# Performance work log

Measured on AMD Instinct MI355X. Metric: run time of the kernel, lower is better.

## Reference

```python
import jax, jax.numpy as jnp
import numpy as np

N, E = 50000, 800000          # nodes, directed edges
IN_DIM, HC, OUT_DIM = 128, 64, 128
NEG_SLOPE = 0.2               # PyG GATConv default leaky_relu slope
EPS = 1e-5                    # PyG LayerNorm default eps


def setup_inputs() -> dict:
    key = jax.random.key(0)
    ks = jax.random.split(key, 10)
    s = 0.1
    return {
        "x": jax.random.normal(ks[0], (N, IN_DIM), jnp.float32),
        "edge_index": jax.random.randint(ks[1], (2, E), 0, N, dtype=jnp.int32),
        # conv1: GATConv(IN_DIM -> HC, heads=2, concat=True)
        "W1": jax.random.normal(ks[2], (IN_DIM, 2 * HC), jnp.float32) * s,
        "att_src1": jax.random.normal(ks[3], (2, HC), jnp.float32) * s,
        "att_dst1": jax.random.normal(ks[4], (2, HC), jnp.float32) * s,
        "b1": jnp.zeros((2 * HC,), jnp.float32),
        "ln1_w": jnp.ones((2 * HC,), jnp.float32),
        "ln1_b": jnp.zeros((2 * HC,), jnp.float32),
        # conv2: GATConv(2*HC -> OUT_DIM, heads=1, concat=False)
        "W2": jax.random.normal(ks[5], (2 * HC, OUT_DIM), jnp.float32) * s,
        "att_src2": jax.random.normal(ks[6], (1, OUT_DIM), jnp.float32) * s,
        "att_dst2": jax.random.normal(ks[7], (1, OUT_DIM), jnp.float32) * s,
        "b2": jnp.zeros((OUT_DIM,), jnp.float32),
        "ln2_w": jnp.ones((OUT_DIM,), jnp.float32),
        "ln2_b": jnp.zeros((OUT_DIM,), jnp.float32),
    }


def gat_conv(x, src, dst, W, att_src, att_dst, bias, heads, C, concat):
    """PyG GATConv (shared lin for src/dst, self-loops already in src/dst)."""
    n = x.shape[0]
    h = (x @ W).reshape(n, heads, C)                       # [N,H,C]
    a_src = jnp.einsum('nhc,hc->nh', h, att_src)           # [N,H]
    a_dst = jnp.einsum('nhc,hc->nh', h, att_dst)           # [N,H]
    e = jax.nn.leaky_relu(a_src[src] + a_dst[dst], NEG_SLOPE)   # [E',H]
    # numerically-stable softmax over incoming edges of each dst node
    emax = jax.ops.segment_max(e, dst, num_segments=n)     # [N,H] (self-loops => non-empty)
    ex = jnp.exp(e - emax[dst])
    denom = jax.ops.segment_sum(ex, dst, num_segments=n)
    alpha = ex / (denom[dst] + 1e-16)                      # [E',H]
    out = jax.ops.segment_sum(h[src] * alpha[:, :, None], dst, num_segments=n)  # [N,H,C]
    out = out.reshape(n, heads * C) if concat else out.mean(axis=1)
    return out + bias


def graph_layernorm(x, w, b):
    """PyG LayerNorm, mode='graph', single graph: normalize over ALL nodes+features."""
    mean = x.mean()
    xc = x - mean
    var = (xc * xc).mean()
    return xc * jax.lax.rsqrt(var + EPS) * w + b


def reference(x, edge_index, W1, att_src1, att_dst1, b1, ln1_w, ln1_b,
              W2, att_src2, att_dst2, b2, ln2_w, ln2_b):
    n = x.shape[0]
    loop = jnp.arange(n, dtype=edge_index.dtype)
    src = jnp.concatenate([edge_index[0], loop])           # add self-loops for GAT convs
    dst = jnp.concatenate([edge_index[1], loop])

    h = gat_conv(x, src, dst, W1, att_src1, att_dst1, b1, heads=2, C=HC, concat=True)
    h = jax.nn.relu(graph_layernorm(h, ln1_w, ln1_b))
    h = gat_conv(h, src, dst, W2, att_src2, att_dst2, b2, heads=1, C=OUT_DIM, concat=False)
    h = graph_layernorm(h, ln2_w, ln2_b)

    # SimpleConv(aggr='mean') over the ORIGINAL edges (no self-loops), then residual
    s0, d0 = edge_index[0], edge_index[1]
    agg = jax.ops.segment_sum(h[s0], d0, num_segments=n)
    cnt = jax.ops.segment_sum(jnp.ones(s0.shape, h.dtype), d0, num_segments=n)
    mean_agg = agg / jnp.maximum(cnt, 1.0)[:, None]
    return jax.nn.relu(mean_agg + x)
```

## Files before the change

### kernel.cpp

```cpp
#include <hip/hip_runtime.h>
#include <hip/hip_bf16.h>
#include <cstdint>
#include <cstddef>

#define NN 50000
#define EE 800000
#define DD 128
#define NEG 0.2f
#define EPSL 1e-5f

#define NB   64
#define EPB  12544
#define NBKT 196
#define HM   (NBKT * NB)
#define SCAP 7168

#define GROWS 64
#define AB    (NN / 8)

typedef __hip_bfloat16 bf16;
typedef short short8 __attribute__((ext_vector_type(8)));
typedef float f32x4 __attribute__((ext_vector_type(4)));

__device__ inline float bflo(unsigned u) { return __uint_as_float(u << 16); }
__device__ inline float bfhi(unsigned u) { return __uint_as_float(u & 0xffff0000u); }
__device__ inline float bf2f(unsigned short u) { return __uint_as_float((unsigned)u << 16); }

__device__ inline unsigned short f2bf(float f) {
    __bf16 h = (__bf16)f;
    return __builtin_bit_cast(unsigned short, h);
}
__device__ inline unsigned pack2(float a, float b) {
    return (unsigned)f2bf(a) | ((unsigned)f2bf(b) << 16);
}

__device__ inline void store4(float* Out, size_t idx, float4 v) {
    *(float4*)&Out[idx] = v;
}
__device__ inline void store4(bf16* Out, size_t idx, float4 v) {
    union { bf16 b[4]; ushort4 u; } cv;
    cv.b[0] = (bf16)v.x; cv.b[1] = (bf16)v.y; cv.b[2] = (bf16)v.z; cv.b[3] = (bf16)v.w;
    *(ushort4*)&Out[idx] = cv.u;
}


__global__ __launch_bounds__(256) void hist_kernel(const int* __restrict__ ei,
                                                   int* __restrict__ histG) {
    __shared__ int lh[NBKT];
    int tid = threadIdx.x;
    for (int t = tid; t < NBKT; t += 256) lh[t] = 0;
    __syncthreads();
    int base = blockIdx.x * EPB;
    #pragma unroll
    for (int j = 0; j < (EPB + 1023) / 1024; ++j) {
        int off = (j * 256 + tid) * 4;
        if (off < EPB) {
            int i4 = base + off;
            if (i4 < EE) {
                int4 d4 = *(const int4*)&ei[EE + i4];
                atomicAdd(&lh[(unsigned)d4.x >> 8], 1);
                atomicAdd(&lh[(unsigned)d4.y >> 8], 1);
                atomicAdd(&lh[(unsigned)d4.z >> 8], 1);
                atomicAdd(&lh[(unsigned)d4.w >> 8], 1);
            }
        }
    }
    __syncthreads();
    for (int t = tid; t < NBKT; t += 256) histG[t * NB + blockIdx.x] = lh[t];
}

__global__ __launch_bounds__(1024) void scan_hist_kernel(const int* __restrict__ histG,
                                                         int* __restrict__ offs,
                                                         int* __restrict__ bstart) {
    __shared__ int wsum[16];
    __shared__ int carry_s;
    int tid = threadIdx.x, lane = tid & 63, wv = tid >> 6;
    if (tid == 0) carry_s = 0;
    __syncthreads();
    for (int base = 0; base < HM; base += 4096) {
        int i4 = base + tid * 4;
        int4 v = make_int4(0, 0, 0, 0);
        if (i4 + 3 < HM) v = *(const int4*)&histG[i4];
        else {
            if (i4 + 0 < HM) v.x = histG[i4 + 0];
            if (i4 + 1 < HM) v.y = histG[i4 + 1];
            if (i4 + 2 < HM) v.z = histG[i4 + 2];
            if (i4 + 3 < HM) v.w = histG[i4 + 3];
        }
        int tsum = v.x + v.y + v.z + v.w;
        int x = tsum;
        for (int off = 1; off < 64; off <<= 1) {
            int t = __shfl_up(x, off);
            if (lane >= off) x += t;
        }
        if (lane == 63) wsum[wv] = x;
        __syncthreads();
        if (wv == 0) {
            int s = (lane < 16) ? wsum[lane] : 0;
            for (int off = 1; off < 16; off <<= 1) {
                int t = __shfl_up(s, off);
                if (lane >= off) s += t;
            }
            if (lane < 16) wsum[lane] = s;
        }
        __syncthreads();
        int waveoff = (wv == 0) ? 0 : wsum[wv - 1];
        int carry = carry_s;
        int o0 = carry + waveoff + x - tsum;
        int o1 = o0 + v.x, o2 = o1 + v.y, o3 = o2 + v.z;
        if (i4 + 3 < HM) *(int4*)&offs[i4] = make_int4(o0, o1, o2, o3);
        else {
            if (i4 + 0 < HM) offs[i4 + 0] = o0;
            if (i4 + 1 < HM) offs[i4 + 1] = o1;
            if (i4 + 2 < HM) offs[i4 + 2] = o2;
            if (i4 + 3 < HM) offs[i4 + 3] = o3;
        }
        if (i4 < HM && (i4 % NB) == 0) bstart[i4 / NB] = o0;
        __syncthreads();
        if (tid == 0) carry_s += wsum[15];
        __syncthreads();
    }
    if (tid == 0) bstart[NBKT] = carry_s;
}

__global__ __launch_bounds__(512) void bucket_sort_kernel(const unsigned* __restrict__ tmp,
                                                          const int* __restrict__ bstart,
                                                          unsigned* __restrict__ col,
                                                          int* __restrict__ row_ptr) {
    __shared__ int cnt[256];
    __shared__ int cpos[256];
    __shared__ int wtot[4];
    __shared__ unsigned stage[SCAP];
    __shared__ unsigned sorted[SCAP];
    int tid = threadIdx.x, lane = tid & 63, wv = tid >> 6;
    int s0 = bstart[blockIdx.x], s1 = bstart[blockIdx.x + 1];
    int cntE = s1 - s0;
    bool lds_ok = (cntE <= SCAP);
    for (int t = tid; t < 256; t += 512) cnt[t] = 0;
    __syncthreads();
    if (lds_ok) {
        for (int i = tid; i < cntE; i += 512) {
            unsigned k = tmp[s0 + i];
            stage[i] = k;
            atomicAdd(&cnt[(k >> 16) & 0xFF], 1);
        }
    } else {
        for (int i = s0 + tid; i < s1; i += 512)
            atomicAdd(&cnt[(tmp[i] >> 16) & 0xFF], 1);
    }
    __syncthreads();
    int v = 0, x = 0;
    if (tid < 256) {
        v = cnt[tid];
        x = v;
        for (int off = 1; off < 64; off <<= 1) {
            int t = __shfl_up(x, off);
            if (lane >= off) x += t;
        }
        if (lane == 63) wtot[wv] = x;
    }
    __syncthreads();
    if (tid < 256) {
        int add = 0;
        for (int k = 0; k < wv; ++k) add += wtot[k];
        int start = s0 + add + x - v;
        cpos[tid] = start;
        int d = blockIdx.x * 256 + tid;
        if (d <= NN) row_ptr[d] = start;
    }
    __syncthreads();
    if (lds_ok) {
        for (int i = tid; i < cntE; i += 512) {
            unsigned key = stage[i];
            int pos = atomicAdd(&cpos[(key >> 16) & 0xFF], 1);
            sorted[pos - s0] = key;
        }
        __syncthreads();
        for (int i = tid; i < cntE; i += 512) col[s0 + i] = sorted[i];
    } else {
        for (int i = s0 + tid; i < s1; i += 512) {
            unsigned key = tmp[i];
            int pos = atomicAdd(&cpos[(key >> 16) & 0xFF], 1);
            col[pos] = key;
        }
    }
}

template <int H, bool LN, typename XT>
__device__ __forceinline__ void gemm_attn_body(int gb,
                                               const XT* __restrict__ X,
                                               const float* __restrict__ W,
                                               const float* __restrict__ att_s,
                                               const float* __restrict__ att_d,
                                               const float2* __restrict__ pstats,
                                               const float* __restrict__ lnw,
                                               const float* __restrict__ lnb,
                                               bf16* __restrict__ Hout,
                                               float* __restrict__ a_src,
                                               float* __restrict__ a_dst) {
    __shared__ __align__(16) char lds[(128 * 136 + 64 * 136) * 2 + 2048];
    unsigned short* Bt = (unsigned short*)lds;
    unsigned short* As = (unsigned short*)(lds + 128 * 136 * 2);
    float* Cs = (float*)lds;
    float* psum = (float*)(lds + (128 * 136 + 64 * 136) * 2);
    __shared__ double w1d[8], w2d[8], sred[2];

    int tid = threadIdx.x;
    int lane = tid & 63, w = tid >> 6;
    int row0 = gb * GROWS;

    double s1 = 0.0, s2 = 0.0;
    if (LN) {
        for (int i = tid; i < AB; i += 512) {
            float2 pv = pstats[i];
            s1 += (double)pv.x; s2 += (double)pv.y;
        }
    }

    {
        int c = tid & 127, kg = tid >> 7;
        #pragma unroll 2
        for (int i = 0; i < 8; ++i) {
            int k0 = i * 16 + kg * 4;
            float wa = W[(size_t)(k0 + 0) * DD + c];
            float wb = W[(size_t)(k0 + 1) * DD + c];
            float wcv = W[(size_t)(k0 + 2) * DD + c];
            float wdv = W[(size_t)(k0 + 3) * DD + c];
            uint2 pk = make_uint2(pack2(wa, wb), pack2(wcv, wdv));
            *(uint2*)&Bt[c * 136 + k0] = pk;
        }
    }

    if (LN) {
        #pragma unroll
        for (int off = 32; off; off >>= 1) {
            s1 += __shfl_xor(s1, off);
            s2 += __shfl_xor(s2, off);
        }
        if (lane == 0) { w1d[w] = s1; w2d[w] = s2; }
    }
    __syncthreads();
    if (LN && tid == 0) {
        double a = 0.0, b = 0.0;
        #pragma unroll
        for (int k = 0; k < 8; ++k) { a += w1d[k]; b += w2d[k]; }
        sred[0] = a; sred[1] = b;
    }
    __syncthreads();

    {
        int sub = tid & 31, rq = tid >> 5;
        int c4 = sub * 4;
        float mean = 0.f, inv = 1.f;
        float4 lw4 = make_float4(1.f, 1.f, 1.f, 1.f), lb4 = make_float4(0.f, 0.f, 0.f, 0.f);
        if (LN) {
            const double M = (double)NN * DD;
            double mean_d = sred[0] / M;
            double var_d = sred[1] / M - mean_d * mean_d;
            mean = (float)mean_d;
            inv = rsqrtf((float)var_d + EPSL);
            lw4 = *(const float4*)&lnw[c4];
            lb4 = *(const float4*)&lnb[c4];
        }
        #pragma unroll
        for (int i = 0; i < 4; ++i) {
            int r = i * 16 + rq;
            int row = row0 + r;
            float4 xv = make_float4(0.f, 0.f, 0.f, 0.f);
            if (row < NN) {
                if constexpr (sizeof(XT) == 4) {
                    xv = *(const float4*)&((const float*)X)[(size_t)row * DD + c4];
                } else {
                    ushort4 xb = *(const ushort4*)&((const unsigned short*)X)[(size_t)row * DD + c4];
                    xv = make_float4(bf2f(xb.x), bf2f(xb.y), bf2f(xb.z), bf2f(xb.w));
                }
            }
            if (LN) {
                xv.x = fmaxf((xv.x - mean) * inv * lw4.x + lb4.x, 0.f);
                xv.y = fmaxf((xv.y - mean) * inv * lw4.y + lb4.y, 0.f);
                xv.z = fmaxf((xv.z - mean) * inv * lw4.z + lb4.z, 0.f);
                xv.w = fmaxf((xv.w - mean) * inv * lw4.w + lb4.w, 0.f);
            }
            uint2 pk = make_uint2(pack2(xv.x, xv.y), pack2(xv.z, xv.w));
            *(uint2*)&As[r * 136 + c4] = pk;
        }
    }
    __syncthreads();

    int rg = w & 3, cg = w >> 2;
    int l15 = lane & 15, quad = lane >> 4;
    f32x4 acc[4];
    #pragma unroll
    for (int t = 0; t < 4; ++t) acc[t] = 0.f;
    const unsigned short* Arow = As + (rg * 16 + l15) * 136 + quad * 8;
    const unsigned short* Brow = Bt + l15 * 136 + quad * 8;
    #pragma unroll
    for (int ks = 0; ks < 4; ++ks) {
        short8 a = *(const short8*)(Arow + ks * 32);
        #pragma unroll
        for (int tt = 0; tt < 4; ++tt) {
            short8 b = *(const short8*)(Brow + (cg * 4 + tt) * 16 * 136 + ks * 32);
            acc[tt] = __builtin_amdgcn_mfma_f32_16x16x32_bf16(a, b, acc[tt], 0, 0, 0);
        }
    }
    __syncthreads();

    #pragma unroll
    for (int tt = 0; tt < 4; ++tt)
        #pragma unroll
        for (int r = 0; r < 4; ++r)
            Cs[(rg * 16 + quad * 4 + r) * 132 + (cg * 4 + tt) * 16 + l15] = acc[tt][r];

    float ds[4] = {0.f, 0.f, 0.f, 0.f}, dd[4] = {0.f, 0.f, 0.f, 0.f};
    #pragma unroll
    for (int tt = 0; tt < 4; ++tt) {
        int cc = (cg * 4 + tt) * 16 + l15;
        float as_ = att_s[cc], ad_ = att_d[cc];
        #pragma unroll
        for (int r = 0; r < 4; ++r) {
            ds[r] = fmaf(acc[tt][r], as_, ds[r]);
            dd[r] = fmaf(acc[tt][r], ad_, dd[r]);
        }
    }
    #pragma unroll
    for (int off = 1; off < 16; off <<= 1) {
        #pragma unroll
        for (int r = 0; r < 4; ++r) {
            ds[r] += __shfl_xor(ds[r], off);
            dd[r] += __shfl_xor(dd[r], off);
        }
    }
    if (l15 == 0) {
        #pragma unroll
        for (int r = 0; r < 4; ++r) {
            int rr = rg * 16 + quad * 4 + r;
            int row = row0 + rr;
            if (H == 2) {
                if (row < NN) {
                    a_src[row * 2 + cg] = ds[r];
                    a_dst[row * 2 + cg] = dd[r];
                }
            } else {
                psum[cg * 64 + rr] = ds[r];
                psum[128 + cg * 64 + rr] = dd[r];
            }
        }
    }
    __syncthreads();

    if (H == 1 && tid < 64) {
        int row = row0 + tid;
        if (row < NN) {
            a_src[row] = psum[tid] + psum[64 + tid];
            a_dst[row] = psum[128 + tid] + psum[192 + tid];
        }
    }

    {
        int sub = tid & 31, rq = tid >> 5;
        int c4 = sub * 4;
        unsigned short* Hp = (unsigned short*)Hout;
        #pragma unroll
        for (int i = 0; i < 4; ++i) {
            int r = i * 16 + rq;
            int row = row0 + r;
            if (row < NN) {
                float4 cv = *(const float4*)&Cs[r * 132 + c4];
                ushort4 pk;
                pk.x = f2bf(cv.x); pk.y = f2bf(cv.y);
                pk.z = f2bf(cv.z); pk.w = f2bf(cv.w);
                *(ushort4*)&Hp[(size_t)row * DD + c4] = pk;
            }
        }
    }
}

template <int H, bool LN, typename XT>
__global__ __launch_bounds__(512) void gemm_attn(const XT* __restrict__ X,
                                                 const float* __restrict__ W,
                                                 const float* __restrict__ att_s,
                                                 const float* __restrict__ att_d,
                                                 const float2* __restrict__ pstats,
                                                 const float* __restrict__ lnw,
                                                 const float* __restrict__ lnb,
                                                 bf16* __restrict__ Hout,
                                                 float* __restrict__ a_src,
                                                 float* __restrict__ a_dst) {
    gemm_attn_body<H, LN, XT>(blockIdx.x, X, W, att_s, att_d, pstats, lnw, lnb,
                              Hout, a_src, a_dst);
}

__global__ __launch_bounds__(512) void scatter_gemm1(const int* __restrict__ ei,
                                                     const int* __restrict__ offs,
                                                     unsigned* __restrict__ tmp,
                                                     const float* __restrict__ X,
                                                     const float* __restrict__ W,
                                                     const float* __restrict__ att_s,
                                                     const float* __restrict__ att_d,
                                                     bf16* __restrict__ Hout,
                                                     float* __restrict__ a_src,
                                                     float* __restrict__ a_dst) {
    if (blockIdx.x < NB) {
        __shared__ int lofs[NBKT];
        int tid = threadIdx.x;
        for (int t = tid; t < NBKT; t += 512) lofs[t] = offs[t * NB + blockIdx.x];
        __syncthreads();
        int base = blockIdx.x * EPB;
        #pragma unroll
        for (int j = 0; j < (EPB + 2047) / 2048; ++j) {
            int off = (j * 512 + tid) * 4;
            if (off < EPB) {
                int i4 = base + off;
                if (i4 < EE) {
                    int4 s4 = *(const int4*)&ei[i4];
                    int4 d4 = *(const int4*)&ei[EE + i4];
                    unsigned k0 = ((unsigned)d4.x << 16) | (unsigned)s4.x;
                    unsigned k1 = ((unsigned)d4.y << 16) | (unsigned)s4.y;
                    unsigned k2 = ((unsigned)d4.z << 16) | (unsigned)s4.z;
                    unsigned k3 = ((unsigned)d4.w << 16) | (unsigned)s4.w;
                    tmp[atomicAdd(&lofs[(unsigned)d4.x >> 8], 1)] = k0;
                    tmp[atomicAdd(&lofs[(unsigned)d4.y >> 8], 1)] = k1;
                    tmp[atomicAdd(&lofs[(unsigned)d4.z >> 8], 1)] = k2;
                    tmp[atomicAdd(&lofs[(unsigned)d4.w >> 8], 1)] = k3;
                }
            }
        }
    } else {
        gemm_attn_body<2, false, float>(blockIdx.x - NB, X, W, att_s, att_d,
                                        nullptr, nullptr, nullptr, Hout, a_src, a_dst);
    }
}

template <int H, typename OT>
__global__ __launch_bounds__(256) void gat_agg(const int* __restrict__ row_ptr,
                                               const unsigned* __restrict__ col,
                                               const bf16* __restrict__ Hin,
                                               const float* __restrict__ a_src,
                                               const float* __restrict__ a_dst,
                                               const float* __restrict__ bias,
                                               OT* __restrict__ Out,
                                               float2* __restrict__ pstats) {
    int tid = threadIdx.x;
    int sl = tid & 31;
    int hw = tid >> 5;
    int n = blockIdx.x * 8 + hw;
    int c0 = sl * 4;
    const int head4 = (H == 2) ? (sl >> 4) : 0;

    int beg = row_ptr[n], end = row_ptr[n + 1];
    int deg = end - beg;

    float ad0 = a_dst[n * H + 0];
    float ad1 = (H == 2) ? a_dst[n * H + 1] : 0.f;
    const ushort* Hp = (const ushort*)Hin + c0;

    float acc[4] = {0.f, 0.f, 0.f, 0.f};
    float dl0 = 0.f, dl1 = 0.f;

    for (int base = 0; base < deg; base += 32) {
        int ecnt = min(32, deg - base);
        int sv = 0; float w0v = 0.f, w1v = 0.f;
        if (sl < ecnt) {
            sv = (int)(col[beg + base + sl] & 0xffffu);
            if (H == 2) {
                float2 av = *(const float2*)&a_src[sv * 2];
                float e0 = av.x + ad0; e0 = (e0 > 0.f) ? e0 : NEG * e0;
                float e1 = av.y + ad1; e1 = (e1 > 0.f) ? e1 : NEG * e1;
                w0v = __expf(e0); w1v = __expf(e1);
                dl0 += w0v; dl1 += w1v;
            } else {
                float e0 = a_src[sv] + ad0; e0 = (e0 > 0.f) ? e0 : NEG * e0;
                w0v = __expf(e0);
                dl0 += w0v;
            }
        }
        int ecnt16 = (ecnt + 15) & ~15;
        for (int j = 0; j < ecnt16; j += 16) {
            int s[16]; uint2 h[16]; float ww[16];
            #pragma unroll
            for (int u = 0; u < 16; ++u) s[u] = __shfl(sv, j + u, 32);
            #pragma unroll
            for (int u = 0; u < 16; ++u) h[u] = *(const uint2*)(Hp + (size_t)s[u] * DD);
            #pragma unroll
            for (int u = 0; u < 16; ++u) {
                if (H == 2) {
                    float a0 = __shfl(w0v, j + u, 32), b0 = __shfl(w1v, j + u, 32);
                    ww[u] = head4 ? b0 : a0;
                } else {
                    ww[u] = __shfl(w0v, j + u, 32);
                }
            }
            #pragma unroll
            for (int u = 0; u < 16; ++u) {
                acc[0] = fmaf(ww[u], bflo(h[u].x), acc[0]);
                acc[1] = fmaf(ww[u], bfhi(h[u].x), acc[1]);
                acc[2] = fmaf(ww[u], bflo(h[u].y), acc[2]);
                acc[3] = fmaf(ww[u], bfhi(h[u].y), acc[3]);
            }
        }
    }

    #pragma unroll
    for (int off = 1; off < 32; off <<= 1) {
        dl0 += __shfl_xor(dl0, off);
        if (H == 2) dl1 += __shfl_xor(dl1, off);
    }

    float e0 = a_src[n * H + 0] + ad0; e0 = (e0 > 0.f) ? e0 : NEG * e0;
    float ws0 = __expf(e0);
    float ws1 = 0.f;
    if (H == 2) {
        float e1 = a_src[n * H + 1] + ad1; e1 = (e1 > 0.f) ? e1 : NEG * e1;
        ws1 = __expf(e1);
    }
    float den = (H == 2 && head4) ? (dl1 + ws1) : (dl0 + ws0);
    float wself = (H == 2 && head4) ? ws1 : ws0;
    float rinv = 1.f / (den + 1e-16f);
    uint2 hs = *(const uint2*)(Hp + (size_t)n * DD);
    float4 bi = *(const float4*)&bias[c0];
    float4 o;
    o.x = fmaf(wself, bflo(hs.x), acc[0]) * rinv + bi.x;
    o.y = fmaf(wself, bfhi(hs.x), acc[1]) * rinv + bi.y;
    o.z = fmaf(wself, bflo(hs.y), acc[2]) * rinv + bi.z;
    o.w = fmaf(wself, bfhi(hs.y), acc[3]) * rinv + bi.w;
    store4(Out, (size_t)n * DD + c0, o);

    float t1 = o.x + o.y + o.z + o.w;
    float t2 = o.x * o.x + o.y * o.y + o.z * o.z + o.w * o.w;
    #pragma unroll
    for (int off = 1; off < 32; off <<= 1) {
        t1 += __shfl_xor(t1, off);
        t2 += __shfl_xor(t2, off);
    }
    __shared__ float2 ps[8];
    if (sl == 0) ps[hw] = make_float2(t1, t2);
    __syncthreads();
    if (tid == 0) {
        float a = 0.f, b = 0.f;
        #pragma unroll
        for (int k = 0; k < 8; ++k) { a += ps[k].x; b += ps[k].y; }
        pstats[blockIdx.x] = make_float2(a, b);
    }
}

__global__ __launch_bounds__(1024) void reduce_stats_kernel(const float2* __restrict__ pstats,
                                                            double* __restrict__ stats) {
    int tid = threadIdx.x, lane = tid & 63, wv = tid >> 6;
    double s1 = 0.0, s2 = 0.0;
    for (int i = tid; i < AB; i += 1024) {
        float2 v = pstats[i];
        s1 += (double)v.x; s2 += (double)v.y;
    }
    for (int off = 32; off; off >>= 1) {
        s1 += __shfl_xor(s1, off);
        s2 += __shfl_xor(s2, off);
    }
    __shared__ double w1[16], w2[16];
    if (lane == 0) { w1[wv] = s1; w2[wv] = s2; }
    __syncthreads();
    if (tid == 0) {
        double a = 0.0, b = 0.0;
        for (int i = 0; i < 16; ++i) { a += w1[i]; b += w2[i]; }
        stats[0] = a; stats[1] = b;
    }
}

__global__ __launch_bounds__(256) void simpleconv_kernel(const int* __restrict__ row_ptr,
                                                         const unsigned* __restrict__ col,
                                                         const bf16* __restrict__ Hin,
                                                         const float* __restrict__ X,
                                                         const double* __restrict__ stats,
                                                         const float* __restrict__ lnw,
                                                         const float* __restrict__ lnb,
                                                         float* __restrict__ Out) {
    int tid = threadIdx.x;
    int sl = tid & 31;
    int n = blockIdx.x * 8 + (tid >> 5);
    int c0 = sl * 4;
    int beg = row_ptr[n], end = row_ptr[n + 1];
    int deg = end - beg;
    const ushort* Hp = (const ushort*)Hin + c0;

    float acc[4] = {0.f, 0.f, 0.f, 0.f};
    for (int base = 0; base < deg; base += 32) {
        int ecnt = min(32, deg - base);
        int sv = 0;
        if (sl < ecnt) sv = (int)(col[beg + base + sl] & 0xffffu);
        int ecnt16 = (ecnt + 15) & ~15;
        for (int j = 0; j < ecnt16; j += 16) {
            int s[16]; uint2 h[16];
            #pragma unroll
            for (int u = 0; u < 16; ++u) s[u] = __shfl(sv, j + u, 32);
            #pragma unroll
            for (int u = 0; u < 16; ++u) h[u] = *(const uint2*)(Hp + (size_t)s[u] * DD);
            #pragma unroll
            for (int u = 0; u < 16; ++u) {
                float ww = (j + u < ecnt) ? 1.f : 0.f;
                acc[0] = fmaf(ww, bflo(h[u].x), acc[0]);
                acc[1] = fmaf(ww, bfhi(h[u].x), acc[1]);
                acc[2] = fmaf(ww, bflo(h[u].y), acc[2]);
                acc[3] = fmaf(ww, bfhi(h[u].y), acc[3]);
            }
        }
    }

    const double M = (double)NN * DD;
    double mean_d = stats[0] / M;
    double var_d = stats[1] / M - mean_d * mean_d;
    float mean2 = (float)mean_d;
    float inv2 = rsqrtf((float)var_d + EPSL);
    float rc = 1.f / (float)((deg > 0) ? deg : 1);
    float4 xr = *(const float4*)&X[(size_t)n * DD + c0];
    float4 o;
    if (deg > 0) {
        float4 lw = *(const float4*)&lnw[c0];
        float4 lb = *(const float4*)&lnb[c0];
        o.x = (acc[0] * rc - mean2) * inv2 * lw.x + lb.x;
        o.y = (acc[1] * rc - mean2) * inv2 * lw.y + lb.y;
        o.z = (acc[2] * rc - mean2) * inv2 * lw.z + lb.z;
        o.w = (acc[3] * rc - mean2) * inv2 * lw.w + lb.w;
    } else {
        o.x = o.y = o.z = o.w = 0.f;
    }
    o.x = fmaxf(o.x + xr.x, 0.f);
    o.y = fmaxf(o.y + xr.y, 0.f);
    o.z = fmaxf(o.z + xr.z, 0.f);
    o.w = fmaxf(o.w + xr.w, 0.f);
    *(float4*)&Out[(size_t)n * DD + c0] = o;
}

extern "C" void kernel_launch(void* const* d_in, const int* in_sizes, int n_in,
                              void* d_out, int out_size, void* d_ws, size_t ws_size,
                              hipStream_t stream) {
    const float* x    = (const float*)d_in[0];
    const int*   ei   = (const int*)d_in[1];
    const float* W1   = (const float*)d_in[2];
    const float* as1  = (const float*)d_in[3];
    const float* ad1  = (const float*)d_in[4];
    const float* b1   = (const float*)d_in[5];
    const float* ln1w = (const float*)d_in[6];
    const float* ln1b = (const float*)d_in[7];
    const float* W2   = (const float*)d_in[8];
    const float* as2  = (const float*)d_in[9];
    const float* ad2  = (const float*)d_in[10];
    const float* b2   = (const float*)d_in[11];
    const float* ln2w = (const float*)d_in[12];
    const float* ln2b = (const float*)d_in[13];
    float* out = (float*)d_out;

    char* p = (char*)d_ws;
    auto alloc = [&](size_t bytes) {
        void* r = (void*)p;
        p += (bytes + 255) & ~(size_t)255;
        return r;
    };
    unsigned* tmp     = (unsigned*)alloc((size_t)EE * 4);
    unsigned* col     = (unsigned*)alloc((size_t)EE * 4);
    int*      histG   = (int*)alloc((size_t)HM * 4);
    int*      offs    = (int*)alloc((size_t)HM * 4);
    int*      bstart  = (int*)alloc((size_t)(NBKT + 1) * 4);
    int*      row_ptr = (int*)alloc((size_t)(NN + 256) * 4);
    double*   stats2  = (double*)alloc(16);
    float2*   pstats  = (float2*)alloc((size_t)AB * 8);
    bf16*     bufA    = (bf16*)alloc((size_t)NN * DD * 2);
    bf16*     bufB    = (bf16*)alloc((size_t)NN * DD * 2);
    float*    aS1     = (float*)alloc((size_t)NN * 2 * 4);
    float*    aD1     = (float*)alloc((size_t)NN * 2 * 4);
    float*    aS2     = (float*)alloc((size_t)NN * 4);
    float*    aD2     = (float*)alloc((size_t)NN * 4);

    const int GB = (NN + GROWS - 1) / GROWS;

    hist_kernel<<<NB, 256, 0, stream>>>(ei, histG);
    scan_hist_kernel<<<1, 1024, 0, stream>>>(histG, offs, bstart);
    scatter_gemm1<<<NB + GB, 512, 0, stream>>>(ei, offs, tmp,
                                               x, W1, as1, ad1, bufA, aS1, aD1);
    bucket_sort_kernel<<<NBKT, 512, 0, stream>>>(tmp, bstart, col, row_ptr);

    gat_agg<2, bf16><<<AB, 256, 0, stream>>>(row_ptr, col, bufA, aS1, aD1, b1, bufB, pstats);

    gemm_attn<1, true, bf16><<<GB, 512, 0, stream>>>(bufB, W2, as2, ad2,
                                                     pstats, ln1w, ln1b,
                                                     bufA, aS2, aD2);
    gat_agg<1, bf16><<<AB, 256, 0, stream>>>(row_ptr, col, bufA, aS2, aD2, b2, bufB, pstats);
    reduce_stats_kernel<<<1, 1024, 0, stream>>>(pstats, stats2);

    simpleconv_kernel<<<AB, 256, 0, stream>>>(row_ptr, col, bufB, x,
                                              stats2, ln2w, ln2b, out);
}
```

Measured before the change: 265.2 us.

## Split aggregation kernels into channel halves with two edges per half-wave

The GAT aggregation and SimpleConv kernels now launch twice as many blocks. Each block covers one 64-channel half of the feature row, and each half-warp processes alternating edges. The two half-warp accumulators are combined with a shuffle at the end. The goal is more memory-level parallelism and occupancy for the gather-heavy edge loops, at the cost of reading the edge list and attention scores twice and doubling the partial-statistics buffer that the LayerNorm reductions consume.

```diff
diff --git a/kernel.cpp b/kernel.cpp
--- a/kernel.cpp
+++ b/kernel.cpp
@@ -211,7 +211,7 @@
 
     double s1 = 0.0, s2 = 0.0;
     if (LN) {
-        for (int i = tid; i < AB; i += 512) {
+        for (int i = tid; i < 2 * AB; i += 512) {
             float2 pv = pstats[i];
             s1 += (double)pv.x; s2 += (double)pv.y;
         }
@@ -443,90 +443,78 @@
     int tid = threadIdx.x;
     int sl = tid & 31;
     int hw = tid >> 5;
-    int n = blockIdx.x * 8 + hw;
-    int c0 = sl * 4;
-    const int head4 = (H == 2) ? (sl >> 4) : 0;
+    int ch = (blockIdx.x < AB) ? 0 : 1;
+    int blk = blockIdx.x - ch * AB;
+    int n = blk * 8 + hw;
+    int half = sl >> 4;
+    int c4 = ch * 64 + (sl & 15) * 4;
 
     int beg = row_ptr[n], end = row_ptr[n + 1];
     int deg = end - beg;
 
-    float ad0 = a_dst[n * H + 0];
-    float ad1 = (H == 2) ? a_dst[n * H + 1] : 0.f;
-    const ushort* Hp = (const ushort*)Hin + c0;
+    float ad = a_dst[n * H + ((H == 2) ? ch : 0)];
+    const ushort* Hp = (const ushort*)Hin + c4;
 
     float acc[4] = {0.f, 0.f, 0.f, 0.f};
-    float dl0 = 0.f, dl1 = 0.f;
+    float dl = 0.f;
 
     for (int base = 0; base < deg; base += 32) {
         int ecnt = min(32, deg - base);
-        int sv = 0; float w0v = 0.f, w1v = 0.f;
+        int sv = 0; float wv = 0.f;
         if (sl < ecnt) {
             sv = (int)(col[beg + base + sl] & 0xffffu);
-            if (H == 2) {
-                float2 av = *(const float2*)&a_src[sv * 2];
-                float e0 = av.x + ad0; e0 = (e0 > 0.f) ? e0 : NEG * e0;
-                float e1 = av.y + ad1; e1 = (e1 > 0.f) ? e1 : NEG * e1;
-                w0v = __expf(e0); w1v = __expf(e1);
-                dl0 += w0v; dl1 += w1v;
-            } else {
-                float e0 = a_src[sv] + ad0; e0 = (e0 > 0.f) ? e0 : NEG * e0;
-                w0v = __expf(e0);
-                dl0 += w0v;
-            }
+            float as_ = (H == 2) ? a_src[sv * 2 + ch] : a_src[sv];
+            float e = as_ + ad; e = (e > 0.f) ? e : NEG * e;
+            wv = __expf(e);
+            dl += wv;
         }
         int ecnt16 = (ecnt + 15) & ~15;
         for (int j = 0; j < ecnt16; j += 16) {
-            int s[16]; uint2 h[16]; float ww[16];
+            int s[8]; uint2 h[8]; float ww[8];
             #pragma unroll
-            for (int u = 0; u < 16; ++u) s[u] = __shfl(sv, j + u, 32);
+            for (int q = 0; q < 8; ++q) s[q] = __shfl(sv, j + 2 * q + half, 32);
             #pragma unroll
-            for (int u = 0; u < 16; ++u) h[u] = *(const uint2*)(Hp + (size_t)s[u] * DD);
+            for (int q = 0; q < 8; ++q) h[q] = *(const uint2*)(Hp + (size_t)s[q] * DD);
             #pragma unroll
-            for (int u = 0; u < 16; ++u) {
-                if (H == 2) {
-                    float a0 = __shfl(w0v, j + u, 32), b0 = __shfl(w1v, j + u, 32);
-                    ww[u] = head4 ? b0 : a0;
-                } else {
-                    ww[u] = __shfl(w0v, j + u, 32);
-                }
-            }
+            for (int q = 0; q < 8; ++q) ww[q] = __shfl(wv, j + 2 * q + half, 32);
             #pragma unroll
-            for (int u = 0; u < 16; ++u) {
-                acc[0] = fmaf(ww[u], bflo(h[u].x), acc[0]);
-                acc[1] = fmaf(ww[u], bfhi(h[u].x), acc[1]);
-                acc[2] = fmaf(ww[u], bflo(h[u].y), acc[2]);
-                acc[3] = fmaf(ww[u], bfhi(h[u].y), acc[3]);
-            }
-        }
-    }
-
-    #pragma unroll
-    for (int off = 1; off < 32; off <<= 1) {
-        dl0 += __shfl_xor(dl0, off);
-        if (H == 2) dl1 += __shfl_xor(dl1, off);
-    }
-
-    float e0 = a_src[n * H + 0] + ad0; e0 = (e0 > 0.f) ? e0 : NEG * e0;
-    float ws0 = __expf(e0);
-    float ws1 = 0.f;
-    if (H == 2) {
-        float e1 = a_src[n * H + 1] + ad1; e1 = (e1 > 0.f) ? e1 : NEG * e1;
-        ws1 = __expf(e1);
-    }
-    float den = (H == 2 && head4) ? (dl1 + ws1) : (dl0 + ws0);
-    float wself = (H == 2 && head4) ? ws1 : ws0;
-    float rinv = 1.f / (den + 1e-16f);
+            for (int q = 0; q < 8; ++q) {
+                acc[0] = fmaf(ww[q], bflo(h[q].x), acc[0]);
+                acc[1] = fmaf(ww[q], bfhi(h[q].x), acc[1]);
+                acc[2] = fmaf(ww[q], bflo(h[q].y), acc[2]);
+                acc[3] = fmaf(ww[q], bfhi(h[q].y), acc[3]);
+            }
+        }
+    }
+
+    #pragma unroll
+    for (int k = 0; k < 4; ++k) acc[k] += __shfl_xor(acc[k], 16, 32);
+
+    #pragma unroll
+    for (int off = 1; off < 32; off <<= 1) dl += __shfl_xor(dl, off);
+
+    float es = a_src[n * H + ((H == 2) ? ch : 0)] + ad;
+    es = (es > 0.f) ? es : NEG * es;
+    float ws = __expf(es);
+    float rinv = 1.f / (dl + ws + 1e-16f);
     uint2 hs = *(const uint2*)(Hp + (size_t)n * DD);
-    float4 bi = *(const float4*)&bias[c0];
-    float4 o;
-    o.x = fmaf(wself, bflo(hs.x), acc[0]) * rinv + bi.x;
-    o.y = fmaf(wself, bfhi(hs.x), acc[1]) * rinv + bi.y;
-    o.z = fmaf(wself, bflo(hs.y), acc[2]) * rinv + bi.z;
-    o.w = fmaf(wself, bfhi(hs.y), acc[3]) * rinv + bi.w;
-    store4(Out, (size_t)n * DD + c0, o);
-
-    float t1 = o.x + o.y + o.z + o.w;
-    float t2 = o.x * o.x + o.y * o.y + o.z * o.z + o.w * o.w;
+    acc[0] = fmaf(ws, bflo(hs.x), acc[0]);
+    acc[1] = fmaf(ws, bfhi(hs.x), acc[1]);
+    acc[2] = fmaf(ws, bflo(hs.y), acc[2]);
+    acc[3] = fmaf(ws, bfhi(hs.y), acc[3]);
+
+    float t1 = 0.f, t2 = 0.f;
+    if (half == 0) {
+        float4 bi = *(const float4*)&bias[c4];
+        float4 o;
+        o.x = acc[0] * rinv + bi.x;
+        o.y = acc[1] * rinv + bi.y;
+        o.z = acc[2] * rinv + bi.z;
+        o.w = acc[3] * rinv + bi.w;
+        store4(Out, (size_t)n * DD + c4, o);
+        t1 = o.x + o.y + o.z + o.w;
+        t2 = o.x * o.x + o.y * o.y + o.z * o.z + o.w * o.w;
+    }
     #pragma unroll
     for (int off = 1; off < 32; off <<= 1) {
         t1 += __shfl_xor(t1, off);
@@ -547,7 +535,7 @@
                                                             double* __restrict__ stats) {
     int tid = threadIdx.x, lane = tid & 63, wv = tid >> 6;
     double s1 = 0.0, s2 = 0.0;
-    for (int i = tid; i < AB; i += 1024) {
+    for (int i = tid; i < 2 * AB; i += 1024) {
         float2 v = pstats[i];
         s1 += (double)v.x; s2 += (double)v.y;
     }
@@ -575,11 +563,15 @@
                                                          float* __restrict__ Out) {
     int tid = threadIdx.x;
     int sl = tid & 31;
-    int n = blockIdx.x * 8 + (tid >> 5);
-    int c0 = sl * 4;
+    int hw = tid >> 5;
+    int ch = (blockIdx.x < AB) ? 0 : 1;
+    int blk = blockIdx.x - ch * AB;
+    int n = blk * 8 + hw;
+    int half = sl >> 4;
+    int c4 = ch * 64 + (sl & 15) * 4;
     int beg = row_ptr[n], end = row_ptr[n + 1];
     int deg = end - beg;
-    const ushort* Hp = (const ushort*)Hin + c0;
+    const ushort* Hp = (const ushort*)Hin + c4;
 
     float acc[4] = {0.f, 0.f, 0.f, 0.f};
     for (int base = 0; base < deg; base += 32) {
@@ -588,45 +580,50 @@
         if (sl < ecnt) sv = (int)(col[beg + base + sl] & 0xffffu);
         int ecnt16 = (ecnt + 15) & ~15;
         for (int j = 0; j < ecnt16; j += 16) {
-            int s[16]; uint2 h[16];
+            int s[8]; uint2 h[8];
             #pragma unroll
-            for (int u = 0; u < 16; ++u) s[u] = __shfl(sv, j + u, 32);
+            for (int q = 0; q < 8; ++q) s[q] = __shfl(sv, j + 2 * q + half, 32);
             #pragma unroll
-            for (int u = 0; u < 16; ++u) h[u] = *(const uint2*)(Hp + (size_t)s[u] * DD);
+            for (int q = 0; q < 8; ++q) h[q] = *(const uint2*)(Hp + (size_t)s[q] * DD);
             #pragma unroll
-            for (int u = 0; u < 16; ++u) {
-                float ww = (j + u < ecnt) ? 1.f : 0.f;
-                acc[0] = fmaf(ww, bflo(h[u].x), acc[0]);
-                acc[1] = fmaf(ww, bfhi(h[u].x), acc[1]);
-                acc[2] = fmaf(ww, bflo(h[u].y), acc[2]);
-                acc[3] = fmaf(ww, bfhi(h[u].y), acc[3]);
-            }
-        }
-    }
-
-    const double M = (double)NN * DD;
-    double mean_d = stats[0] / M;
-    double var_d = stats[1] / M - mean_d * mean_d;
-    float mean2 = (float)mean_d;
-    float inv2 = rsqrtf((float)var_d + EPSL);
-    float rc = 1.f / (float)((deg > 0) ? deg : 1);
-    float4 xr = *(const float4*)&X[(size_t)n * DD + c0];
-    float4 o;
-    if (deg > 0) {
-        float4 lw = *(const float4*)&lnw[c0];
-        float4 lb = *(const float4*)&lnb[c0];
-        o.x = (acc[0] * rc - mean2) * inv2 * lw.x + lb.x;
-        o.y = (acc[1] * rc - mean2) * inv2 * lw.y + lb.y;
-        o.z = (acc[2] * rc - mean2) * inv2 * lw.z + lb.z;
-        o.w = (acc[3] * rc - mean2) * inv2 * lw.w + lb.w;
-    } else {
-        o.x = o.y = o.z = o.w = 0.f;
-    }
-    o.x = fmaxf(o.x + xr.x, 0.f);
-    o.y = fmaxf(o.y + xr.y, 0.f);
-    o.z = fmaxf(o.z + xr.z, 0.f);
-    o.w = fmaxf(o.w + xr.w, 0.f);
-    *(float4*)&Out[(size_t)n * DD + c0] = o;
+            for (int q = 0; q < 8; ++q) {
+                float ww = (j + 2 * q + half < ecnt) ? 1.f : 0.f;
+                acc[0] = fmaf(ww, bflo(h[q].x), acc[0]);
+                acc[1] = fmaf(ww, bfhi(h[q].x), acc[1]);
+                acc[2] = fmaf(ww, bflo(h[q].y), acc[2]);
+                acc[3] = fmaf(ww, bfhi(h[q].y), acc[3]);
+            }
+        }
+    }
+
+    #pragma unroll
+    for (int k = 0; k < 4; ++k) acc[k] += __shfl_xor(acc[k], 16, 32);
+
+    if (half == 0) {
+        const double M = (double)NN * DD;
+        double mean_d = stats[0] / M;
+        double var_d = stats[1] / M - mean_d * mean_d;
+        float mean2 = (float)mean_d;
+        float inv2 = rsqrtf((float)var_d + EPSL);
+        float rc = 1.f / (float)((deg > 0) ? deg : 1);
+        float4 xr = *(const float4*)&X[(size_t)n * DD + c4];
+        float4 o;
+        if (deg > 0) {
+            float4 lw = *(const float4*)&lnw[c4];
+            float4 lb = *(const float4*)&lnb[c4];
+            o.x = (acc[0] * rc - mean2) * inv2 * lw.x + lb.x;
+            o.y = (acc[1] * rc - mean2) * inv2 * lw.y + lb.y;
+            o.z = (acc[2] * rc - mean2) * inv2 * lw.z + lb.z;
+            o.w = (acc[3] * rc - mean2) * inv2 * lw.w + lb.w;
+        } else {
+            o.x = o.y = o.z = o.w = 0.f;
+        }
+        o.x = fmaxf(o.x + xr.x, 0.f);
+        o.y = fmaxf(o.y + xr.y, 0.f);
+        o.z = fmaxf(o.z + xr.z, 0.f);
+        o.w = fmaxf(o.w + xr.w, 0.f);
+        *(float4*)&Out[(size_t)n * DD + c4] = o;
+    }
 }
 
 extern "C" void kernel_launch(void* const* d_in, const int* in_sizes, int n_in,
@@ -661,7 +658,7 @@
     int*      bstart  = (int*)alloc((size_t)(NBKT + 1) * 4);
     int*      row_ptr = (int*)alloc((size_t)(NN + 256) * 4);
     double*   stats2  = (double*)alloc(16);
-    float2*   pstats  = (float2*)alloc((size_t)AB * 8);
+    float2*   pstats  = (float2*)alloc((size_t)2 * AB * 8);
     bf16*     bufA    = (bf16*)alloc((size_t)NN * DD * 2);
     bf16*     bufB    = (bf16*)alloc((size_t)NN * DD * 2);
     float*    aS1     = (float*)alloc((size_t)NN * 2 * 4);
@@ -677,14 +674,16 @@
                                                x, W1, as1, ad1, bufA, aS1, aD1);
     bucket_sort_kernel<<<NBKT, 512, 0, stream>>>(tmp, bstart, col, row_ptr);
 
-    gat_agg<2, bf16><<<AB, 256, 0, stream>>>(row_ptr, col, bufA, aS1, aD1, b1, bufB, pstats);
+    gat_agg<2, bf16><<<2 * AB, 256, 0, stream>>>(row_ptr, col, bufA, aS1, aD1, b1,
+                                                 bufB, pstats);
 
     gemm_attn<1, true, bf16><<<GB, 512, 0, stream>>>(bufB, W2, as2, ad2,
                                                      pstats, ln1w, ln1b,
                                                      bufA, aS2, aD2);
-    gat_agg<1, bf16><<<AB, 256, 0, stream>>>(row_ptr, col, bufA, aS2, aD2, b2, bufB, pstats);
+    gat_agg<1, bf16><<<2 * AB, 256, 0, stream>>>(row_ptr, col, bufA, aS2, aD2, b2,
+                                                 bufB, pstats);
     reduce_stats_kernel<<<1, 1024, 0, stream>>>(pstats, stats2);
 
-    simpleconv_kernel<<<AB, 256, 0, stream>>>(row_ptr, col, bufB, x,
-                                              stats2, ln2w, ln2b, out);
-}
+    simpleconv_kernel<<<2 * AB, 256, 0, stream>>>(row_ptr, col, bufB, x,
+                                                  stats2, ln2w, ln2b, out);
+}
```

Result: slower. 270.9 us (+2.1%).
